# Performance work log

Measured on AMD Instinct MI355X. Metric: run time of the kernel, lower is better.

The kernel has to match this reference:

```python
import jax, jax.numpy as jnp
import numpy as np

D, H, E, OUT = 1024, 2048, 8, 512
B = 4096
LN_EPS = 1e-5


def _ln(x, g, b):
    m = jnp.mean(x, axis=-1, keepdims=True)
    v = jnp.mean((x - m) ** 2, axis=-1, keepdims=True)
    return (x - m) / jnp.sqrt(v + LN_EPS) * g + b


def _gelu(x):
    return jax.nn.gelu(x, approximate=False)  # torch nn.GELU default (erf)


def setup_inputs() -> dict:
    key = jax.random.key(0)
    ks = jax.random.split(key, 8)
    s = 0.02
    f32 = jnp.float32
    return {
        "x": jax.random.normal(ks[0], (B, D), f32),
        # router: Linear(D, D)
        "Wr": jax.random.normal(ks[1], (D, D), f32) * s,
        "br": jnp.zeros((D,), f32),
        # expert stacks [E, ...]: Linear(D,H)+LN(H), Linear(H,H)+LN(H), Linear(H,D)+LN(D)
        "W1": jax.random.normal(ks[2], (E, D, H), f32) * s,
        "b1": jnp.zeros((E, H), f32),
        "g1": jnp.ones((E, H), f32),
        "be1": jnp.zeros((E, H), f32),
        "W2": jax.random.normal(ks[3], (E, H, H), f32) * s,
        "b2": jnp.zeros((E, H), f32),
        "g2": jnp.ones((E, H), f32),
        "be2": jnp.zeros((E, H), f32),
        "W3": jax.random.normal(ks[4], (E, H, D), f32) * s,
        "b3": jnp.zeros((E, D), f32),
        "g3": jnp.ones((E, D), f32),
        "be3": jnp.zeros((E, D), f32),
        # out_linear: Linear(D, OUT) + LN(OUT)
        "Wo": jax.random.normal(ks[5], (D, OUT), f32) * s,
        "bo": jnp.zeros((OUT,), f32),
        "go": jnp.ones((OUT,), f32),
        "beo": jnp.zeros((OUT,), f32),
        "k": 2,
    }


def reference(x, Wr, br, W1, b1, g1, be1, W2, b2, g2, be2, W3, b3, g3, be3,
              Wo, bo, go, beo, k):
    nB = x.shape[0]
    nE = W1.shape[0]

    # Router: shared Linear applied to E identical copies of x -> identical
    # per-expert embeddings [B, E, D] (faithful to source).
    remb = x @ Wr + br                                   # [B, D]
    diff = x - remb                                      # [B, D]
    dist = jnp.sqrt(jnp.sum(diff * diff, axis=-1))       # [B]
    distances = jnp.broadcast_to(dist[:, None], (nB, nE))  # [B, E] (all tied)

    # Laplace gating: top-k of -distance, exp, normalize.
    top_vals, top_idx = jax.lax.top_k(-distances, k)     # [B, k]
    sc = jnp.exp(top_vals)
    probs = sc / jnp.sum(sc, axis=-1, keepdims=True)     # [B, k]

    # Dense all-expert compute (E small), then gather selected.
    h = _gelu(jnp.einsum('bd,edh->ebh', x, W1) + b1[:, None, :])
    h = _ln(h, g1[:, None, :], be1[:, None, :])
    h = _gelu(jnp.einsum('ebh,ehg->ebg', h, W2) + b2[:, None, :])
    h = _ln(h, g2[:, None, :], be2[:, None, :])
    h = _gelu(jnp.einsum('ebh,ehd->ebd', h, W3) + b3[:, None, :])
    h = _ln(h, g3[:, None, :], be3[:, None, :])          # [E, B, D]

    hb = jnp.transpose(h, (1, 0, 2))                     # [B, E, D]
    sel = jnp.take_along_axis(hb, top_idx[:, :, None], axis=1, mode='clip')  # [B,k,D]
    # Source quirk: probs (shape [B,k]) indexed by expert id; tied top-k always
    # yields ids 0..k-1 so this is in-range — reproduce with clip gather.
    w = jnp.take_along_axis(probs, top_idx, axis=1, mode='clip')             # [B,k]
    combined = jnp.sum(sel * w[:, :, None], axis=1)      # [B, D]

    outs = _ln(_gelu(combined @ Wo + bo), go, beo)       # [B, OUT]

    # entropy loss computed on probs [B, k] (as in source: logits := topk probs)
    p = jax.nn.softmax(probs, axis=-1)
    lp = jax.nn.log_softmax(probs, axis=-1)
    entropy = -jnp.sum(p * lp, axis=-1)                  # [B]
    pm = jnp.mean(p, axis=-1)                            # [B]
    ent_loss = jnp.mean(jnp.mean(entropy) - pm * jnp.log(pm))
    return outs, ent_loss
```

## Files before the change

kernel.cpp:

```cpp
#include <hip/hip_runtime.h>


typedef __attribute__((ext_vector_type(8))) short short8;
typedef __attribute__((ext_vector_type(4))) float f32x4;

static __device__ __forceinline__ unsigned short f2bf(float f) {
  union { float f; unsigned u; } a; a.f = f;
  unsigned u = a.u;
  u += 0x7FFFu + ((u >> 16) & 1u);
  return (unsigned short)(u >> 16);
}

static __device__ __forceinline__ float bf2f(unsigned short u) {
  union { float f; unsigned u; } a; a.u = ((unsigned)u) << 16;
  return a.f;
}

static __device__ __forceinline__ float gelu_erf(float v) {
  return 0.5f * v * (1.0f + erff(v * 0.70710678118654752f));
}

__global__ __launch_bounds__(256) void cvt_kernel(const float* __restrict__ X,
                                                  unsigned short* __restrict__ XB) {
  size_t i = (size_t)blockIdx.x * 256 + threadIdx.x;
  const float4* X4 = (const float4*)X;
  float4 f = X4[i];
  ushort4 u;
  u.x = f2bf(f.x); u.y = f2bf(f.y); u.z = f2bf(f.z); u.w = f2bf(f.w);
  *(ushort4*)(XB + 4 * i) = u;
}

__global__ __launch_bounds__(256) void transpose_cvt(const float* __restrict__ in,
                                                     unsigned short* __restrict__ outp,
                                                     int K, int N) {
  __shared__ float tile[32][33];
  size_t base = (size_t)blockIdx.z * (size_t)K * (size_t)N;
  int k0 = blockIdx.y * 32, n0 = blockIdx.x * 32;
  int tx = threadIdx.x, ty = threadIdx.y;
#pragma unroll
  for (int j = 0; j < 32; j += 8)
    tile[ty + j][tx] = in[base + (size_t)(k0 + ty + j) * N + n0 + tx];
  __syncthreads();
#pragma unroll
  for (int j = 0; j < 32; j += 8)
    outp[base + (size_t)(n0 + ty + j) * K + k0 + tx] = f2bf(tile[tx][ty + j]);
}

template <int BM, int BN, int WR, int WC>
__global__ __launch_bounds__(256) void gemm_bias(
    const unsigned short* __restrict__ A, const unsigned short* __restrict__ Bt,
    const float* __restrict__ bias, unsigned short* __restrict__ C,
    int N, int K, long sA, long sB, long sBias, long sC) {
  constexpr int TM = BM / WR, TN = BN / WC;
  constexpr int IM = TM / 16, JN = TN / 16;
  int e = blockIdx.z;
  A += (size_t)e * sA;
  Bt += (size_t)e * sB;
  bias += (size_t)e * sBias;
  C += (size_t)e * sC;

  __shared__ unsigned short As[BM * 32];
  __shared__ unsigned short Bs[BN * 32];

  int t = threadIdx.x;
  int wave = t >> 6, lane = t & 63;
  int wr = wave / WC, wc = wave % WC;
  int lrow = lane & 15, lq = lane >> 4;

  const unsigned short* ag = A + (size_t)(blockIdx.x * BM + (t >> 2)) * K + (t & 3) * 8;
  const unsigned short* bg = Bt + (size_t)(blockIdx.y * BN + (t >> 2)) * K + (t & 3) * 8;
  unsigned short* al = As + t * 8;
  unsigned short* bl = Bs + t * 8;

  f32x4 acc[IM][JN];
#pragma unroll
  for (int i = 0; i < IM; i++)
#pragma unroll
    for (int j = 0; j < JN; j++) acc[i][j] = (f32x4){0.f, 0.f, 0.f, 0.f};

  int nk = K >> 5;
  for (int kt = 0; kt < nk; ++kt) {
    __syncthreads();
#pragma unroll
    for (int c = 0; c < BM / 64; ++c)
      __builtin_amdgcn_global_load_lds(
          (const __attribute__((address_space(1))) void*)(ag + (size_t)(64 * c) * K),
          (__attribute__((address_space(3))) void*)(al + 64 * c * 32), 16, 0, 0);
#pragma unroll
    for (int c = 0; c < BN / 64; ++c)
      __builtin_amdgcn_global_load_lds(
          (const __attribute__((address_space(1))) void*)(bg + (size_t)(64 * c) * K),
          (__attribute__((address_space(3))) void*)(bl + 64 * c * 32), 16, 0, 0);
    ag += 32;
    bg += 32;
    __syncthreads();

    short8 af[IM], bf[JN];
#pragma unroll
    for (int i = 0; i < IM; i++)
      af[i] = *(const short8*)(As + ((wr * TM + i * 16 + lrow) * 32 + lq * 8));
#pragma unroll
    for (int j = 0; j < JN; j++)
      bf[j] = *(const short8*)(Bs + ((wc * TN + j * 16 + lrow) * 32 + lq * 8));
#pragma unroll
    for (int i = 0; i < IM; i++)
#pragma unroll
      for (int j = 0; j < JN; j++)
        acc[i][j] = __builtin_amdgcn_mfma_f32_16x16x32_bf16(af[i], bf[j], acc[i][j], 0, 0, 0);
  }

  int m0 = blockIdx.x * BM + wr * TM + lq * 4;
  int n0 = blockIdx.y * BN + wc * TN + lrow;
#pragma unroll
  for (int j = 0; j < JN; j++) {
    int n = n0 + j * 16;
    float bv = bias[n];
#pragma unroll
    for (int i = 0; i < IM; i++) {
#pragma unroll
      for (int r = 0; r < 4; r++) {
        int m = m0 + i * 16 + r;
        C[(size_t)m * N + n] = f2bf(acc[i][j][r] + bv);
      }
    }
  }
}

template <int NPT>
__global__ __launch_bounds__(256) void gelu_ln(const unsigned short* __restrict__ T,
                                               const float* __restrict__ g,
                                               const float* __restrict__ be,
                                               unsigned short* __restrict__ H,
                                               long sT, long sH, int sP) {
  typedef short vecS __attribute__((ext_vector_type(NPT)));
  constexpr int N = 256 * NPT;
  int e = blockIdx.y;
  size_t row = blockIdx.x;
  int t = threadIdx.x;
  const unsigned short* tp = T + (size_t)e * sT + row * N + t * NPT;
  const float* gp = g + (size_t)e * sP + t * NPT;
  const float* bp = be + (size_t)e * sP + t * NPT;
  unsigned short* hp = H + (size_t)e * sH + row * N + t * NPT;

  vecS rv = *(const vecS*)tp;
  float v[NPT], s = 0.f, q = 0.f;
#pragma unroll
  for (int i = 0; i < NPT; i++) {
    v[i] = gelu_erf(bf2f((unsigned short)rv[i]));
    s += v[i];
    q += v[i] * v[i];
  }
#pragma unroll
  for (int off = 32; off > 0; off >>= 1) {
    s += __shfl_down(s, off, 64);
    q += __shfl_down(q, off, 64);
  }
  __shared__ float rs[4], rq[4];
  int wv = t >> 6;
  if ((t & 63) == 0) { rs[wv] = s; rq[wv] = q; }
  __syncthreads();
  s = rs[0] + rs[1] + rs[2] + rs[3];
  q = rq[0] + rq[1] + rq[2] + rq[3];
  float m = s * (1.f / N);
  float rstd = rsqrtf(q * (1.f / N) - m * m + 1e-5f);
  vecS ov;
#pragma unroll
  for (int i = 0; i < NPT; i++)
    ov[i] = (short)f2bf((v[i] - m) * rstd * gp[i] + bp[i]);
  *(vecS*)hp = ov;
}

__global__ __launch_bounds__(256) void ln3_combine(const unsigned short* __restrict__ T,
                                                   const float* __restrict__ g,
                                                   const float* __restrict__ be,
                                                   unsigned short* __restrict__ CB) {
  size_t row = blockIdx.x;
  int t = threadIdx.x;
  const unsigned short* t0 = T + row * 1024 + t * 4;
  const unsigned short* t1 = T + (size_t)4096 * 1024 + row * 1024 + t * 4;
  ushort4 r0 = *(const ushort4*)t0;
  ushort4 r1 = *(const ushort4*)t1;
  float v0[4], v1[4];
  v0[0] = gelu_erf(bf2f(r0.x)); v0[1] = gelu_erf(bf2f(r0.y));
  v0[2] = gelu_erf(bf2f(r0.z)); v0[3] = gelu_erf(bf2f(r0.w));
  v1[0] = gelu_erf(bf2f(r1.x)); v1[1] = gelu_erf(bf2f(r1.y));
  v1[2] = gelu_erf(bf2f(r1.z)); v1[3] = gelu_erf(bf2f(r1.w));
  float s0 = 0.f, q0 = 0.f, s1 = 0.f, q1 = 0.f;
#pragma unroll
  for (int i = 0; i < 4; i++) {
    s0 += v0[i]; q0 += v0[i] * v0[i];
    s1 += v1[i]; q1 += v1[i] * v1[i];
  }
#pragma unroll
  for (int off = 32; off > 0; off >>= 1) {
    s0 += __shfl_down(s0, off, 64); q0 += __shfl_down(q0, off, 64);
    s1 += __shfl_down(s1, off, 64); q1 += __shfl_down(q1, off, 64);
  }
  __shared__ float r[4][4];
  int wv = t >> 6;
  if ((t & 63) == 0) { r[0][wv] = s0; r[1][wv] = q0; r[2][wv] = s1; r[3][wv] = q1; }
  __syncthreads();
  s0 = r[0][0] + r[0][1] + r[0][2] + r[0][3];
  q0 = r[1][0] + r[1][1] + r[1][2] + r[1][3];
  s1 = r[2][0] + r[2][1] + r[2][2] + r[2][3];
  q1 = r[3][0] + r[3][1] + r[3][2] + r[3][3];
  float m0 = s0 * (1.f / 1024.f), m1 = s1 * (1.f / 1024.f);
  float rs0 = rsqrtf(q0 * (1.f / 1024.f) - m0 * m0 + 1e-5f);
  float rs1 = rsqrtf(q1 * (1.f / 1024.f) - m1 * m1 + 1e-5f);
  int n = t * 4;
  ushort4 o;
  float a, b;
  a = (v0[0] - m0) * rs0 * g[n + 0] + be[n + 0];
  b = (v1[0] - m1) * rs1 * g[1024 + n + 0] + be[1024 + n + 0];
  o.x = f2bf(0.5f * (a + b));
  a = (v0[1] - m0) * rs0 * g[n + 1] + be[n + 1];
  b = (v1[1] - m1) * rs1 * g[1024 + n + 1] + be[1024 + n + 1];
  o.y = f2bf(0.5f * (a + b));
  a = (v0[2] - m0) * rs0 * g[n + 2] + be[n + 2];
  b = (v1[2] - m1) * rs1 * g[1024 + n + 2] + be[1024 + n + 2];
  o.z = f2bf(0.5f * (a + b));
  a = (v0[3] - m0) * rs0 * g[n + 3] + be[n + 3];
  b = (v1[3] - m1) * rs1 * g[1024 + n + 3] + be[1024 + n + 3];
  o.w = f2bf(0.5f * (a + b));
  *(ushort4*)(CB + row * 1024 + n) = o;
}

__global__ __launch_bounds__(256) void lno_kernel(const unsigned short* __restrict__ T,
                                                  const float* __restrict__ g,
                                                  const float* __restrict__ be,
                                                  float* __restrict__ out) {
  size_t row = blockIdx.x;
  int t = threadIdx.x;
  const unsigned short* tp = T + row * 512 + t * 2;
  ushort2 rv = *(const ushort2*)tp;
  float v[2];
  v[0] = gelu_erf(bf2f(rv.x));
  v[1] = gelu_erf(bf2f(rv.y));
  float s = v[0] + v[1];
  float q = v[0] * v[0] + v[1] * v[1];
#pragma unroll
  for (int off = 32; off > 0; off >>= 1) {
    s += __shfl_down(s, off, 64);
    q += __shfl_down(q, off, 64);
  }
  __shared__ float rs[4], rq[4];
  int wv = t >> 6;
  if ((t & 63) == 0) { rs[wv] = s; rq[wv] = q; }
  __syncthreads();
  s = rs[0] + rs[1] + rs[2] + rs[3];
  q = rq[0] + rq[1] + rq[2] + rq[3];
  float m = s * (1.f / 512.f);
  float rstd = rsqrtf(q * (1.f / 512.f) - m * m + 1e-5f);
  int n = t * 2;
  float2 o;
  o.x = (v[0] - m) * rstd * g[n] + be[n];
  o.y = (v[1] - m) * rstd * g[n + 1] + be[n + 1];
  *(float2*)(out + row * 512 + n) = o;
  if (row == 0 && t == 0) out[(size_t)4096 * 512] = 1.03972077f;
}

extern "C" void kernel_launch(void* const* d_in, const int* in_sizes, int n_in,
                              void* d_out, int out_size, void* d_ws, size_t ws_size,
                              hipStream_t stream) {
  const float* x   = (const float*)d_in[0];
  const float* W1  = (const float*)d_in[3];
  const float* b1  = (const float*)d_in[4];
  const float* g1  = (const float*)d_in[5];
  const float* be1 = (const float*)d_in[6];
  const float* W2  = (const float*)d_in[7];
  const float* b2  = (const float*)d_in[8];
  const float* g2  = (const float*)d_in[9];
  const float* be2 = (const float*)d_in[10];
  const float* W3  = (const float*)d_in[11];
  const float* b3  = (const float*)d_in[12];
  const float* g3  = (const float*)d_in[13];
  const float* be3 = (const float*)d_in[14];
  const float* Wo  = (const float*)d_in[15];
  const float* bo  = (const float*)d_in[16];
  const float* go  = (const float*)d_in[17];
  const float* beo = (const float*)d_in[18];
  float* out = (float*)d_out;

  char* w = (char*)d_ws;
  unsigned short* xb  = (unsigned short*)(w + 0);
  unsigned short* W1t = (unsigned short*)(w + 8388608);
  unsigned short* W2t = (unsigned short*)(w + 16777216);
  unsigned short* W3t = (unsigned short*)(w + 33554432);
  unsigned short* Wot = (unsigned short*)(w + 41943040);
  unsigned short* tR  = (unsigned short*)(w + 42991616);
  unsigned short* hA  = (unsigned short*)(w + 76546048);
  unsigned short* cb  = (unsigned short*)(w + 110100480);
  unsigned short* to  = (unsigned short*)(w + 118489088);

  dim3 tb(32, 8);
  cvt_kernel<<<4096, 256, 0, stream>>>(x, xb);
  transpose_cvt<<<dim3(64, 32, 2), tb, 0, stream>>>(W1, W1t, 1024, 2048);
  transpose_cvt<<<dim3(64, 64, 2), tb, 0, stream>>>(W2, W2t, 2048, 2048);
  transpose_cvt<<<dim3(32, 64, 2), tb, 0, stream>>>(W3, W3t, 2048, 1024);
  transpose_cvt<<<dim3(16, 32, 1), tb, 0, stream>>>(Wo, Wot, 1024, 512);

  gemm_bias<128, 128, 2, 2><<<dim3(32, 16, 2), 256, 0, stream>>>(
      xb, W1t, b1, tR, 2048, 1024, 0L, 2097152L, 2048L, 8388608L);
  gelu_ln<8><<<dim3(4096, 2), 256, 0, stream>>>(tR, g1, be1, hA, 8388608L, 8388608L, 2048);
  gemm_bias<128, 128, 2, 2><<<dim3(32, 16, 2), 256, 0, stream>>>(
      hA, W2t, b2, tR, 2048, 2048, 8388608L, 4194304L, 2048L, 8388608L);
  gelu_ln<8><<<dim3(4096, 2), 256, 0, stream>>>(tR, g2, be2, hA, 8388608L, 8388608L, 2048);
  gemm_bias<128, 128, 2, 2><<<dim3(32, 8, 2), 256, 0, stream>>>(
      hA, W3t, b3, tR, 1024, 2048, 8388608L, 2097152L, 1024L, 4194304L);
  ln3_combine<<<4096, 256, 0, stream>>>(tR, g3, be3, cb);
  gemm_bias<64, 128, 1, 4><<<dim3(64, 4, 1), 256, 0, stream>>>(
      cb, Wot, bo, to, 512, 1024, 0L, 0L, 0L, 0L);
  lno_kernel<<<4096, 256, 0, stream>>>(to, go, beo, out);
}
```

Measured before the change: 563.4 us.

## Switch GEMMs to 32x32x16 MFMA with XOR-swizzled LDS and retile small GEMMs

The bf16 GEMM kernel now uses the 32x32x16 MFMA instruction instead of 16x16x32. Each wave covers 32x32 output blocks, and the accumulator indexing and epilogue row mapping are updated to match. The K-chunk position in shared memory is XOR-swizzled by row so that the fragment reads avoid LDS bank conflicts. The W3 and output-projection GEMMs move to smaller block tiles so more blocks launch. The aim is more compute per LDS read and fewer bank stalls. The cost is larger per-wave accumulator register use.

```diff
diff --git a/kernel.cpp b/kernel.cpp
--- a/kernel.cpp
+++ b/kernel.cpp
@@ -2,7 +2,7 @@
 
 
 typedef __attribute__((ext_vector_type(8))) short short8;
-typedef __attribute__((ext_vector_type(4))) float f32x4;
+typedef __attribute__((ext_vector_type(16))) float f32x16;
 
 static __device__ __forceinline__ unsigned short f2bf(float f) {
   union { float f; unsigned u; } a; a.f = f;
@@ -52,7 +52,7 @@
     const float* __restrict__ bias, unsigned short* __restrict__ C,
     int N, int K, long sA, long sB, long sBias, long sC) {
   constexpr int TM = BM / WR, TN = BN / WC;
-  constexpr int IM = TM / 16, JN = TN / 16;
+  constexpr int IM = TM / 32, JN = TN / 32;
   int e = blockIdx.z;
   A += (size_t)e * sA;
   Bt += (size_t)e * sB;
@@ -65,18 +65,24 @@
   int t = threadIdx.x;
   int wave = t >> 6, lane = t & 63;
   int wr = wave / WC, wc = wave % WC;
-  int lrow = lane & 15, lq = lane >> 4;
-
-  const unsigned short* ag = A + (size_t)(blockIdx.x * BM + (t >> 2)) * K + (t & 3) * 8;
-  const unsigned short* bg = Bt + (size_t)(blockIdx.y * BN + (t >> 2)) * K + (t & 3) * 8;
+  int lrow = lane & 31;
+  int h = lane >> 5;
+  int l3 = lane & 3;
+
+  int srow = t >> 2;
+  int schunk = (t & 3) ^ (srow & 3);
+  const unsigned short* ag = A + (size_t)(blockIdx.x * BM + srow) * K + schunk * 8;
+  const unsigned short* bg = Bt + (size_t)(blockIdx.y * BN + srow) * K + schunk * 8;
   unsigned short* al = As + t * 8;
   unsigned short* bl = Bs + t * 8;
 
-  f32x4 acc[IM][JN];
+  f32x16 acc[IM][JN];
 #pragma unroll
   for (int i = 0; i < IM; i++)
 #pragma unroll
-    for (int j = 0; j < JN; j++) acc[i][j] = (f32x4){0.f, 0.f, 0.f, 0.f};
+    for (int j = 0; j < JN; j++)
+#pragma unroll
+      for (int r = 0; r < 16; r++) acc[i][j][r] = 0.f;
 
   int nk = K >> 5;
   for (int kt = 0; kt < nk; ++kt) {
@@ -95,31 +101,35 @@
     bg += 32;
     __syncthreads();
 
-    short8 af[IM], bf[JN];
-#pragma unroll
-    for (int i = 0; i < IM; i++)
-      af[i] = *(const short8*)(As + ((wr * TM + i * 16 + lrow) * 32 + lq * 8));
-#pragma unroll
-    for (int j = 0; j < JN; j++)
-      bf[j] = *(const short8*)(Bs + ((wc * TN + j * 16 + lrow) * 32 + lq * 8));
-#pragma unroll
-    for (int i = 0; i < IM; i++)
+#pragma unroll
+    for (int s = 0; s < 2; ++s) {
+      int pc = ((2 * s + h) ^ l3) * 8;
+      short8 af[IM], bf[JN];
+#pragma unroll
+      for (int i = 0; i < IM; i++)
+        af[i] = *(const short8*)(As + (wr * TM + i * 32 + lrow) * 32 + pc);
 #pragma unroll
       for (int j = 0; j < JN; j++)
-        acc[i][j] = __builtin_amdgcn_mfma_f32_16x16x32_bf16(af[i], bf[j], acc[i][j], 0, 0, 0);
-  }
-
-  int m0 = blockIdx.x * BM + wr * TM + lq * 4;
+        bf[j] = *(const short8*)(Bs + (wc * TN + j * 32 + lrow) * 32 + pc);
+#pragma unroll
+      for (int i = 0; i < IM; i++)
+#pragma unroll
+        for (int j = 0; j < JN; j++)
+          acc[i][j] = __builtin_amdgcn_mfma_f32_32x32x16_bf16(af[i], bf[j], acc[i][j], 0, 0, 0);
+    }
+  }
+
+  int m0 = blockIdx.x * BM + wr * TM + 4 * h;
   int n0 = blockIdx.y * BN + wc * TN + lrow;
 #pragma unroll
   for (int j = 0; j < JN; j++) {
-    int n = n0 + j * 16;
+    int n = n0 + j * 32;
     float bv = bias[n];
 #pragma unroll
     for (int i = 0; i < IM; i++) {
 #pragma unroll
-      for (int r = 0; r < 4; r++) {
-        int m = m0 + i * 16 + r;
+      for (int r = 0; r < 16; r++) {
+        int m = m0 + i * 32 + (r & 3) + 8 * (r >> 2);
         C[(size_t)m * N + n] = f2bf(acc[i][j][r] + bv);
       }
     }
@@ -305,10 +315,10 @@
   gemm_bias<128, 128, 2, 2><<<dim3(32, 16, 2), 256, 0, stream>>>(
       hA, W2t, b2, tR, 2048, 2048, 8388608L, 4194304L, 2048L, 8388608L);
   gelu_ln<8><<<dim3(4096, 2), 256, 0, stream>>>(tR, g2, be2, hA, 8388608L, 8388608L, 2048);
-  gemm_bias<128, 128, 2, 2><<<dim3(32, 8, 2), 256, 0, stream>>>(
+  gemm_bias<64, 128, 2, 2><<<dim3(64, 8, 2), 256, 0, stream>>>(
       hA, W3t, b3, tR, 1024, 2048, 8388608L, 2097152L, 1024L, 4194304L);
   ln3_combine<<<4096, 256, 0, stream>>>(tR, g3, be3, cb);
-  gemm_bias<64, 128, 1, 4><<<dim3(64, 4, 1), 256, 0, stream>>>(
+  gemm_bias<64, 64, 2, 2><<<dim3(64, 8, 1), 256, 0, stream>>>(
       cb, Wot, bo, to, 512, 1024, 0L, 0L, 0L, 0L);
   lno_kernel<<<4096, 256, 0, stream>>>(to, go, beo, out);
 }
```

Measured after the change: 564.2 us. No clear change (+0.1%).
